# Kernel tuning notes

Measured on AMD Instinct MI355X. Metric: run time of the kernel, lower is better.

The kernel has to match this reference:

```python
import jax, jax.numpy as jnp
import numpy as np

SC = 19          # window stride/size (non-kitti)
K = 3 * SC       # 57, unfold kernel size
CH = 128         # chnn

def conv2d(x, w, b=None, pad=(0, 0)):
    y = jax.lax.conv_general_dilated(
        x, w, (1, 1), [(pad[0], pad[0]), (pad[1], pad[1])],
        dimension_numbers=('NCHW', 'OIHW', 'NCHW'))
    return y if b is None else y + b[None, :, None, None]

def unfold(x):
    # nn.Unfold(kernel_size=3*SC, padding=SC, stride=SC) -> [b, c, K*K, h_sc*w_sc]
    b, c, h, w = x.shape
    h_sc, w_sc = h // SC, w // SC
    xp = jnp.pad(x, ((0, 0), (0, 0), (SC, SC), (SC, SC)))
    ii = np.arange(h_sc)[:, None] * SC + np.arange(K)[None, :]
    jj = np.arange(w_sc)[:, None] * SC + np.arange(K)[None, :]
    p = xp[:, :, ii, :][:, :, :, :, jj]              # [b,c,h_sc,K,w_sc,K]
    return p.transpose(0, 1, 3, 5, 2, 4).reshape(b, c, K * K, h_sc * w_sc)

def to_windows(x):
    # [b,c,h,w] -> [b,c,h_sc*w_sc, SC*SC] (non-overlapping SCxSC windows)
    b, c, h, w = x.shape
    h_sc, w_sc = h // SC, w // SC
    return x.reshape(b, c, h_sc, SC, w_sc, SC).transpose(0, 1, 2, 4, 3, 5).reshape(b, c, h_sc * w_sc, SC * SC)

def fs_kernel(w_prelu, b, h, w):
    # geometric falloff kernel, separable in x/y: [b, K*K, L, SC*SC]
    a = w_prelu[0] * 0.02      # scp = 0.02
    half = 2.0 * SC            # half_ker
    crd = jnp.arange(K, dtype=jnp.float32)
    idx_x = SC + jnp.arange(w, dtype=jnp.float32) % SC
    idx_y = SC + jnp.arange(h, dtype=jnp.float32) % SC
    def falloff(d):
        v = d - half
        pre = jnp.where(v > 0, v, a * v)   # PReLU
        return jnp.maximum(1.0 - pre, 0.0) # -prelu + b(=1), clamped at 0
    ox = falloff(jnp.abs(crd[:, None] - idx_x[None, :]))  # [K, w]
    oy = falloff(jnp.abs(crd[:, None] - idx_y[None, :]))  # [K, h]
    ker = oy[:, None, :, None] * ox[None, :, None, :]      # [Ky, Kx, h, w]
    ker = jnp.broadcast_to(ker[None], (b, K, K, h, w)).reshape(b, K * K, h, w)
    return to_windows(ker)

def kpa(feat_ci, feat_mi, w_qk, w_v, gamma, w_prelu):
    b, c, h_in, w_in = feat_mi.shape
    x_pad = SC - w_in % SC
    y_pad = SC - h_in % SC
    pad4 = ((0, 0), (0, 0), (0, y_pad), (0, x_pad))
    feat_c = jnp.pad(feat_ci, pad4)
    feat_m = jnp.pad(feat_mi, pad4)
    h, w = h_in + y_pad, w_in + x_pad
    h_sc, w_sc = h // SC, w // SC
    # validity mask -> additive -99 bias for padded keys/queries
    fm = jnp.pad(jnp.ones((1, 1, h_in, w_in), feat_mi.dtype), pad4)
    fm_k = unfold(fm)                                  # [1,1,K^2,L]
    fm_q = to_windows(fm)                              # [1,1,L,SC^2]
    am = (fm_k[:, 0, :, :, None] * fm_q[:, 0, None, :, :] - 1.0) * 99.0
    # itr == 0 path: compute attention
    qk = conv2d(feat_c, w_qk)
    feat_q, feat_k = qk[:, :c], qk[:, c:]
    feat_k = unfold(feat_k) * (c ** -0.5)              # [b,c,K^2,L]
    feat_q = to_windows(feat_q)                        # [b,c,L,SC^2]
    attn = jnp.einsum('bckn,bcns->bkns', feat_k, feat_q) + am
    attn = jax.nn.softmax(fs_kernel(w_prelu, b, h, w) * attn, axis=1)
    feat_v = unfold(conv2d(feat_m, w_v))               # [b,c,K^2,L]
    feat_r = jnp.einsum('bkns,bckn->bcns', attn, feat_v)  # [b,c,L,SC^2]
    feat_r = feat_r.reshape(b, c, h_sc, w_sc, SC, SC).transpose(0, 1, 2, 4, 3, 5).reshape(b, c, h, w)
    return feat_mi + feat_r[:, :, :h_in, :w_in] * gamma[0]

def sep_conv_gru(h, x, wz1, bz1, wr1, br1, wq1, bq1, wz2, bz2, wr2, br2, wq2, bq2):
    hx = jnp.concatenate([h, x], 1)
    z = jax.nn.sigmoid(conv2d(hx, wz1, bz1, (0, 2)))
    r = jax.nn.sigmoid(conv2d(hx, wr1, br1, (0, 2)))
    q = jnp.tanh(conv2d(jnp.concatenate([r * h, x], 1), wq1, bq1, (0, 2)))
    h = (1 - z) * h + z * q
    hx = jnp.concatenate([h, x], 1)
    z = jax.nn.sigmoid(conv2d(hx, wz2, bz2, (2, 0)))
    r = jax.nn.sigmoid(conv2d(hx, wr2, br2, (2, 0)))
    q = jnp.tanh(conv2d(jnp.concatenate([r * h, x], 1), wq2, bq2, (2, 0)))
    return (1 - z) * h + z * q

PARAM_SHAPES = [
    ('w_cor1', (256, 324, 1, 1)), ('b_cor1', (256,)), ('w_cor2', (192, 256, 3, 3)), ('b_cor2', (192,)),
    ('w_flo1', (128, 2, 7, 7)), ('b_flo1', (128,)), ('w_flo2', (64, 128, 3, 3)), ('b_flo2', (64,)),
    ('w_mo', (126, 256, 3, 3)), ('b_mo', (126,)),
    ('w_qk', (256, 128, 1, 1)), ('w_v', (128, 128, 1, 1)),
    ('wz1', (128, 512, 1, 5)), ('bz1', (128,)), ('wr1', (128, 512, 1, 5)), ('br1', (128,)),
    ('wq1', (128, 512, 1, 5)), ('bq1', (128,)),
    ('wz2', (128, 512, 5, 1)), ('bz2', (128,)), ('wr2', (128, 512, 5, 1)), ('br2', (128,)),
    ('wq2', (128, 512, 5, 1)), ('bq2', (128,)),
    ('w_f1', (256, 128, 3, 3)), ('b_f1', (256,)), ('w_f2', (2, 256, 3, 3)), ('b_f2', (2,)),
    ('w_m1', (256, 128, 3, 3)), ('b_m1', (256,)), ('w_m2', (576, 256, 1, 1)), ('b_m2', (576,)),
]

def setup_inputs() -> dict:
    key = jax.random.key(0)
    B, H, W = 2, 55, 128
    ks = jax.random.split(key, len(PARAM_SHAPES) + 4)
    inp = {
        'net': jax.random.normal(ks[0], (B, CH, H, W), jnp.float32),
        'inp': jax.random.normal(ks[1], (B, CH, H, W), jnp.float32),
        'corr': jax.random.normal(ks[2], (B, 324, H, W), jnp.float32),
        'flow': jax.random.normal(ks[3], (B, 2, H, W), jnp.float32),
    }
    for i, (name, shp) in enumerate(PARAM_SHAPES):
        fan_in = int(np.prod(shp[1:])) if len(shp) > 1 else shp[0]
        scale = 1.0 / np.sqrt(fan_in) if len(shp) > 1 else 0.01
        inp[name] = scale * jax.random.normal(ks[4 + i], shp, jnp.float32)
    inp['gamma'] = jnp.array([0.5], jnp.float32)            # nonzero so KPA contributes
    inp['w_prelu'] = jnp.array([1.0 / 28.0], jnp.float32)    # 1 / h_k, h_k = (3*SC-1)/2
    inp['itr'] = 0
    return inp

def reference(net, inp, corr, flow, w_cor1, b_cor1, w_cor2, b_cor2, w_flo1, b_flo1, w_flo2, b_flo2, w_mo, b_mo, w_qk, w_v, wz1, bz1, wr1, br1, wq1, bq1, wz2, bz2, wr2, br2, wq2, bq2, w_f1, b_f1, w_f2, b_f2, w_m1, b_m1, w_m2, b_m2, gamma, w_prelu, itr):
    # _mo_enc
    fc = jax.nn.relu(conv2d(corr, w_cor1, b_cor1))
    fc = jax.nn.relu(conv2d(fc, w_cor2, b_cor2, (1, 1)))
    ff = jax.nn.relu(conv2d(flow, w_flo1, b_flo1, (3, 3)))
    ff = jax.nn.relu(conv2d(ff, w_flo2, b_flo2, (1, 1)))
    fm = jax.nn.relu(conv2d(jnp.concatenate([fc, ff], 1), w_mo, b_mo, (1, 1)))
    feat_mo = jnp.concatenate([fm, flow], 1)           # [b,128,h,w]
    # KPA attention (itr == 0)
    feat_moa = kpa(inp, feat_mo, w_qk, w_v, gamma, w_prelu)
    x = jnp.concatenate([inp, feat_mo, feat_moa], 1)   # [b,384,h,w]
    net = sep_conv_gru(net, x, wz1, bz1, wr1, br1, wq1, bq1, wz2, bz2, wr2, br2, wq2, bq2)
    d = jax.nn.relu(conv2d(net, w_f1, b_f1, (1, 1)))
    delta_flow = conv2d(d, w_f2, b_f2, (1, 1))
    m = jax.nn.relu(conv2d(net, w_m1, b_m1, (1, 1)))
    mask = 0.25 * conv2d(m, w_m2, b_m2)
    return net, mask, delta_flow
```

## Files before the change

kernel.cpp:

```cpp
#include <hip/hip_runtime.h>
#include <hip/hip_bf16.h>

typedef __bf16 bf16;
typedef __attribute__((ext_vector_type(8))) __bf16 v8bf;
typedef __attribute__((ext_vector_type(4))) float f32x4;
typedef __attribute__((ext_vector_type(16))) float f32x16;

#define HH 55
#define WW 128
#define HWP 7040
#define BHW 14080
#define QS 0.08838834764831845f
#define LOG2E 1.4426950408889634f

__device__ __forceinline__ void g2l16(const bf16* g, bf16* l){
  __builtin_amdgcn_global_load_lds(
      (const __attribute__((address_space(1))) void*)g,
      (__attribute__((address_space(3))) void*)l, 16, 0, 0);
}

#define NCV 17
__device__ const int PK_CinSrc[NCV] = {324,256,128,256,128,128,512,512,512,512,512,512,128,128,256,256,98};
__device__ const int PK_Kc[NCV]     = {384,256,128,256,128,128,512,512,512,512,512,512,128,128,256,256,128};
__device__ const int PK_ntap[NCV]   = {1,9,9,9,1,1,5,5,5,5,5,5,9,9,9,1,1};
__device__ const int PK_Ctot[NCV]   = {256,256,128,128,256,128,256,256,128,256,256,128,512,512,128,640,128};
__device__ const int PK_coB[NCV]    = {0,0,0,0,0,0,0,128,0,0,128,0,0,256,0,0,0};
__device__ const int PK_dst[NCV]    = {0,98304,688128,835584,1130496,1163264,1179648,1179648,
  1835008,2162688,2162688,2818048,3145728,3145728,3735552,4030464,4194304};
__device__ const int PKD_cum[NCV+1] = {0,98304,540672,614400,904704,937472,953856,
  1281536,1609216,1936896,2264576,2592256,2919936,3214848,3509760,3514368,3661824,3678208};
__device__ const int PKD_Co[NCV]    = {256,192,64,126,256,128,128,128,128,128,128,128,256,256,2,576,128};

__device__ const int PB_off[15]={0,256,512,640,1152,1280,1408,1536,1664,1792,1920,2176,2432,2560,3200};
__device__ const int PB_cnt[15]={256,192,64,126,128,128,128,128,128,128,256,256,2,576,128};

struct W17 { const float* w[17]; };
struct B15 { const float* b[15]; };

struct XP {
  W17 wp; B15 bp;
  const float *net, *inp, *corr, *flow;
  bf16 *Bp; float *bias;
  bf16 *hx; float *hcur; bf16 *corr_cl; bf16 *im2c;
};

__global__ __launch_bounds__(256) void init_k(XP X){
  __shared__ float T[64][65];
  int bid = blockIdx.x;
  const int t = threadIdx.x;
  if (bid < 14368){
    int idx = bid*256 + t;
    int c = 0;
    while (idx >= PKD_cum[c+1]) ++c;
    int local = idx - PKD_cum[c];
    if (c == 16){
      int co = local >> 7, k = local & 127;
      if (k < 98)
        X.Bp[PK_dst[16] + co*128 + k] = (bf16)X.wp.w[16][co*98 + (k&1)*49 + (k>>1)];
      return;
    }
    int Kc = PK_Kc[c];
    int CKc = PKD_Co[c]*Kc;
    int tap = local / CKc;
    int rem = local - tap*CKc;
    int co = rem / Kc;
    int ci = rem - co*Kc;
    int cs = PK_CinSrc[c];
    if (ci < cs){
      float v = X.wp.w[c][(co*cs + ci)*PK_ntap[c] + tap];
      if (c == 4 && co < 128) v *= QS;
      X.Bp[PK_dst[c] + (tap*PK_Ctot[c] + PK_coB[c] + co)*Kc + ci] = (bf16)v;
    }
    return;
  }
  bid -= 14368;
  if (bid < 880){
    int pt = bid%110, ct = (bid/110)&3, b = bid/440;
    const float* src = (ct < 2) ? X.net : X.inp;
    int c0s = (ct & 1)*64;
    int cbase = (ct < 2) ? 0 : 128;
    int p0 = pt*64;
    int pj = t & 63, cr4 = t >> 6;
#pragma unroll
    for (int i=0;i<16;++i)
      T[cr4 + i*4][pj] = src[((size_t)b*128 + c0s + cr4 + i*4)*HWP + p0 + pj];
    __syncthreads();
    int cj = t & 63, pr4 = t >> 6;
#pragma unroll
    for (int i=0;i<16;++i){
      int pp = p0 + pr4 + i*4;
      float v = T[cj][pr4 + i*4];
      X.hx[((size_t)(b*HWP+pp))*512 + cbase + c0s + cj] = (bf16)v;
      if (ct < 2) X.hcur[((size_t)(b*HWP+pp))*128 + c0s + cj] = v;
    }
    return;
  }
  bid -= 880;
  if (bid < 1320){
    int pt = bid%110, ct = (bid/110)%6, b = bid/660;
    int p0 = pt*64, c0s = ct*64;
    int pj = t & 63, cr4 = t >> 6;
#pragma unroll
    for (int i=0;i<16;++i){
      int c = c0s + cr4 + i*4;
      float v = 0.f;
      if (c < 324) v = X.corr[((size_t)b*324 + c)*HWP + p0 + pj];
      T[cr4 + i*4][pj] = v;
    }
    __syncthreads();
    int cj = t & 63, pr4 = t >> 6;
#pragma unroll
    for (int i=0;i<16;++i){
      int pp = p0 + pr4 + i*4;
      int cc = c0s + cj;
      X.corr_cl[((size_t)(b*HWP+pp))*384 + cc] = (bf16)T[cj][pr4 + i*4];
    }
    return;
  }
  bid -= 1320;
  if (bid < 110){
    int i = bid*256 + t;
    int c = i & 1, p = i >> 1;
    int b = p / HWP, pix = p - b*HWP;
    X.hx[(size_t)p*512 + 382 + c] = (bf16)X.flow[(b*2+c)*HWP + pix];
    return;
  }
  bid -= 110;
  if (bid < 7040){
    int i = bid*256 + t;
    int k = i & 127, p = i >> 7;
    int b = p / HWP, pix = p - b*HWP, y = pix >> 7, x = pix & 127;
    float v = 0.f;
    if (k < 98){
      int tap = k >> 1, c2 = k & 1, kh = tap/7, kw = tap - 7*(tap/7);
      int yy = y + kh - 3, xx = x + kw - 3;
      if ((unsigned)yy < 55u && (unsigned)xx < 128u) v = X.flow[(b*2+c2)*HWP + yy*128 + xx];
    }
    X.im2c[i] = (bf16)v;
    return;
  }
  for (int e=0;e<15;++e)
    for (int o=t; o<PB_cnt[e]; o+=256)
      X.bias[PB_off[e]+o] = X.bp.b[e][o];
}

__global__ __launch_bounds__(256) void transp_v(
    const bf16* __restrict__ src, bf16* __restrict__ dst)
{
  int pt = blockIdx.x, ct = blockIdx.y, b = blockIdx.z;
  __shared__ unsigned short T[64][66];
  int t = threadIdx.x;
  int p0 = pt*64, c0s = ct*64;
  int cj = t & 63, pr4 = t >> 6;
#pragma unroll
  for (int i=0;i<16;++i){
    int pp = p0 + pr4 + i*4;
    T[cj][pr4 + i*4] = ((const unsigned short*)src)[((size_t)(b*HWP+pp))*128 + c0s + cj];
  }
  __syncthreads();
  int pj = t & 63, cr4 = t >> 6;
#pragma unroll
  for (int i=0;i<16;++i){
    int cc = c0s + cr4 + i*4;
    ((unsigned short*)dst)[((size_t)(b*128 + cc))*HWP + p0 + pj] = T[cr4 + i*4][pj];
  }
}

struct GP {
  const bf16* A; const bf16* A2;
  const bf16* Bp; const float* bias;
  void* outp; const float* auxZ; float* auxH; float* auxN;
  int Astride, A2stride, Asplit;
  int outCtot, outC0, Nvalid, Kc, CtotPad, tapcode, act, outmode, ntiles, ntOff;
  float scale;
};

__global__ __launch_bounds__(256) void gemm_conv(GP ga, GP gb, const bf16* __restrict__ zp)
{
  const int Mt = blockIdx.x;
  int nt = blockIdx.y;
  const bool useB = (nt >= ga.ntiles);
  if (useB) nt -= ga.ntiles;
  const bf16* A        = useB ? gb.A : ga.A;
  const bf16* A2       = useB ? gb.A2 : ga.A2;
  const bf16* Bp       = useB ? gb.Bp : ga.Bp;
  const float* bias    = useB ? gb.bias : ga.bias;
  void* outp           = useB ? gb.outp : ga.outp;
  const float* auxZ    = useB ? gb.auxZ : ga.auxZ;
  float* auxH          = useB ? gb.auxH : ga.auxH;
  float* auxN          = useB ? gb.auxN : ga.auxN;
  const int Astride    = useB ? gb.Astride : ga.Astride;
  const int A2stride   = useB ? gb.A2stride : ga.A2stride;
  const int Asplit     = useB ? gb.Asplit : ga.Asplit;
  const int outCtot    = useB ? gb.outCtot : ga.outCtot;
  const int outC0      = useB ? gb.outC0 : ga.outC0;
  const int Nvalid     = useB ? gb.Nvalid : ga.Nvalid;
  const int Kc         = useB ? gb.Kc : ga.Kc;
  const int CtotPad    = useB ? gb.CtotPad : ga.CtotPad;
  const int tapcode    = useB ? gb.tapcode : ga.tapcode;
  const int act        = useB ? gb.act : ga.act;
  const int outmode    = useB ? gb.outmode : ga.outmode;
  const int ntOff      = useB ? gb.ntOff : ga.ntOff;
  const float scale    = useB ? gb.scale : ga.scale;

  const int bimg = Mt/110;
  const int rem = Mt - bimg*110;
  const int yy0 = rem >> 1;
  const int xh  = (rem & 1) << 6;
  const int tid = threadIdx.x;
  const int lane = tid & 63, wave = tid >> 6;
  const int wm = wave >> 1, wn = wave & 1;
  const int lr = lane & 15, lq2 = lane >> 4;

  __shared__ __align__(16) bf16 Al[2][4096];
  __shared__ __align__(16) bf16 Bl[2][8192];

  f32x4 acc[2][4];
#pragma unroll
  for (int m=0;m<2;++m)
#pragma unroll
    for (int n=0;n<4;++n) acc[m][n] = (f32x4){0.f,0.f,0.f,0.f};

  const int ntap = (tapcode==0) ? 1 : (tapcode==1 ? 9 : 5);
  const int nsteps = ntap*(Kc>>6);

  const int srow = tid >> 3;
  const int sc   = tid & 7;

#define STAGE(BUF, T, KC) { \
    int ddy, ddx; \
    if (tapcode==0){ ddy=0; ddx=0; } \
    else if (tapcode==1){ ddy=(T)/3-1; ddx=(T)-3*((T)/3)-1; } \
    else if (tapcode==2){ ddy=0; ddx=(T)-2; } \
    else { ddy=(T)-2; ddx=0; } \
    int ysrc = yy0 + ddy; \
    bool yok = (unsigned)ysrc < 55u; \
    const bf16* Abase; int Astr; \
    if ((KC) < Asplit){ Astr = A2stride; \
      Abase = A2 + (size_t)((bimg*55+ysrc)*128)*Astr + (KC); } \
    else { Astr = Astride; \
      Abase = A + (size_t)((bimg*55+ysrc)*128)*Astr + (KC); } \
    _Pragma("unroll") \
    for (int is=0; is<2; ++is){ \
      int r = is*32 + srow; \
      int cc = sc ^ (r&7); \
      int gx = xh + r + ddx; \
      const bf16* srcp = (yok && (unsigned)gx < 128u) ? \
          (Abase + (size_t)gx*Astr + cc*8) : (zp + cc*8); \
      g2l16(srcp, &Al[BUF][is*2048 + wave*512]); \
    } \
    const bf16* Bt = Bp + (size_t)((T)*CtotPad + (nt+ntOff)*128)*Kc + (KC); \
    _Pragma("unroll") \
    for (int is=0; is<4; ++is){ \
      int r = is*32 + srow; \
      int cc = sc ^ (r&7); \
      g2l16(Bt + (size_t)r*Kc + cc*8, &Bl[BUF][is*2048 + wave*512]); \
    } }

  STAGE(0, 0, 0);
  __syncthreads();

  int tcur = 0, kcc = 0;
  for (int si=0; si<nsteps; ++si){
    int kn = kcc + 64, tn = tcur;
    if (kn == Kc){ kn = 0; tn = tcur + 1; }
    if (si + 1 < nsteps){ STAGE((si+1)&1, tn, kn); }
    __builtin_amdgcn_sched_barrier(0);
    kcc = kn; tcur = tn;
    const bf16* Ac = Al[si&1];
    const bf16* Bc = Bl[si&1];
#pragma unroll
    for (int kk=0; kk<2; ++kk){
      v8bf af[2], bfr[4];
#pragma unroll
      for (int m=0;m<2;++m){
        int row = wm*32 + m*16 + lr;
        af[m] = *(const v8bf*)(Ac + row*64 + (((kk*4+lq2) ^ (row&7))<<3));
      }
#pragma unroll
      for (int n=0;n<4;++n){
        int row = wn*64 + n*16 + lr;
        bfr[n] = *(const v8bf*)(Bc + row*64 + (((kk*4+lq2) ^ (row&7))<<3));
      }
#pragma unroll
      for (int m=0;m<2;++m)
#pragma unroll
        for (int n=0;n<4;++n)
          acc[m][n] = __builtin_amdgcn_mfma_f32_16x16x32_bf16(af[m], bfr[n], acc[m][n], 0,0,0);
    }
    __syncthreads();
  }
#undef STAGE

  const size_t pixbase = (size_t)(bimg*55 + yy0)*128 + xh;
  if (outmode == 0){
    bf16* Ost = (bf16*)Al;
#pragma unroll
    for (int nn=0; nn<4; ++nn){
      int colL = wn*64 + nn*16 + lr;
      float bvl = bias[(nt+ntOff)*128 + colL];
#pragma unroll
      for (int m=0;m<2;++m){
        int rowx = wm*32 + m*16 + lq2*4;
        f32x4 v = acc[m][nn];
#pragma unroll
        for (int r=0;r<4;++r){
          float vv = v[r] + bvl;
          if (act==1)      vv = fmaxf(vv, 0.f);
          else if (act==2) vv = 1.f/(1.f+__expf(-vv));
          else if (act==3) vv = tanhf(vv);
          vv *= scale;
          int row = rowx + r;
          int pch = (colL>>3) ^ (row & 7);
          Ost[row*128 + (pch<<3) + (colL&7)] = (bf16)vv;
        }
      }
    }
    __syncthreads();
    {
      int rowl = tid >> 2, seg = tid & 3;
      size_t p = pixbase + rowl;
      bf16* dstp = (bf16*)outp + p*outCtot + outC0 + (nt+ntOff)*128 + seg*32;
      const bf16* srcr = Ost + rowl*128;
      int cb = (nt+ntOff)*128 + seg*32;
#pragma unroll
      for (int k2=0;k2<4;++k2){
        int pch = (seg*4 + k2) ^ (rowl & 7);
        int cog = cb + k2*8;
        if (cog + 8 <= Nvalid)
          *(uint4*)(dstp + k2*8) = *(const uint4*)(srcr + (pch<<3));
        else if (cog < Nvalid){
          const bf16* s8 = srcr + (pch<<3);
          for (int e=0; e<Nvalid-cog; ++e) dstp[k2*8+e] = s8[e];
        }
      }
    }
  } else if (outmode == 2){
    float* Ost2 = (float*)Bl;
#pragma unroll
    for (int nn=0; nn<4; ++nn){
      int chL = wn*64 + nn*16 + lr;
      float bvl = bias[(nt+ntOff)*128 + chL];
#pragma unroll
      for (int m=0;m<2;++m){
        int rowx = wm*32 + m*16 + lq2*4;
        f32x4 v = acc[m][nn];
#pragma unroll
        for (int r=0;r<4;++r){
          float vv = v[r] + bvl;
          if (act==1)      vv = fmaxf(vv, 0.f);
          else if (act==2) vv = 1.f/(1.f+__expf(-vv));
          else if (act==3) vv = tanhf(vv);
          Ost2[chL*64 + rowx + r] = vv*scale;
        }
      }
    }
    __syncthreads();
    {
      int ch = tid >> 1, half = tid & 1;
      int cog = (nt+ntOff)*128 + ch;
      if (cog < Nvalid){
        float* dstp = (float*)outp + ((size_t)bimg*outCtot + outC0 + cog)*HWP
                    + yy0*128 + xh + half*32;
        const float* srcr = Ost2 + ch*64 + half*32;
#pragma unroll
        for (int k2=0;k2<8;++k2)
          *(uint4*)(dstp + k2*4) = *(const uint4*)(srcr + k2*4);
      }
    }
  } else {
#pragma unroll
    for (int nn=0; nn<4; ++nn){
      int cog = (nt+ntOff)*128 + wn*64 + nn*16 + lr;
      float bvl = bias[cog];
      bool cok = cog < Nvalid;
#pragma unroll
      for (int m=0;m<2;++m){
        int rowx = wm*32 + m*16 + lq2*4;
        f32x4 v = acc[m][nn];
#pragma unroll
        for (int r=0;r<4;++r){
          float vv = v[r] + bvl;
          if (act==1)      vv = fmaxf(vv, 0.f);
          else if (act==2) vv = 1.f/(1.f+__expf(-vv));
          else if (act==3) vv = tanhf(vv);
          vv *= scale;
          if (cok){
            int prow = rowx + r;
            size_t p = pixbase + prow;
            if (outmode==1) ((float*)outp)[p*outCtot + outC0 + cog] = vv;
            else if (outmode==3){
              int c = cog & 127;
              ((bf16*)outp)[p*128 + c] = (bf16)(vv * auxH[p*128 + c]);
            } else {
              int c = cog;
              float z  = auxZ[p*128 + c];
              float h0 = auxH[p*128 + c];
              float hn = (1.f - z)*h0 + z*vv;
              auxH[p*128 + c] = hn;
              ((bf16*)outp)[p*512 + c] = (bf16)hn;
              if (auxN){
                int pixloc = (int)(p - (size_t)bimg*HWP);
                auxN[((size_t)bimg*128 + c)*HWP + pixloc] = hn;
              }
            }
          }
        }
      }
    }
  }
}

__global__ __launch_bounds__(256) void gemm_n16(
    const bf16* __restrict__ A, int Astride,
    const bf16* __restrict__ Bp, const float* __restrict__ bias,
    float* __restrict__ outp, int outCtot, int Kc, int CtotPad)
{
  const int Mt = blockIdx.x;
  const int bimg = Mt/110;
  const int rem = Mt - bimg*110;
  const int yy0 = rem >> 1;
  const int xh  = (rem & 1) << 6;
  const int tid = threadIdx.x;
  const int wave = tid >> 6, lane = tid & 63;
  const int lr = lane & 15, lq2 = lane >> 4;

  __shared__ __align__(16) bf16 Al[4][2560];
  __shared__ __align__(16) bf16 Bl[4][640];
  __shared__ float Rd[4][1024];

  bf16* Alw = Al[wave];
  bf16* Blw = Bl[wave];

  f32x4 acc[4];
#pragma unroll
  for (int m=0;m<4;++m) acc[m] = (f32x4){0.f,0.f,0.f,0.f};

  const int brw = lane >> 2, bc = lane & 3;
  uint4 av[4]; uint4 bv;

#define PFN(SI) { \
    int T_ = (SI) >> 3, KC = ((SI)&7)*32; \
    int ddy = T_/3 - 1, ddx = T_ - 3*(T_/3) - 1; \
    int ysrc = yy0 + ddy; int gx = xh + lane + ddx; \
    bool ok = (unsigned)ysrc < 55u && (unsigned)gx < 128u; \
    const bf16* Ap = A + (size_t)((bimg*55+ysrc)*128 + gx)*Astride + KC; \
    av[0] = ok ? *(const uint4*)(Ap)      : make_uint4(0,0,0,0); \
    av[1] = ok ? *(const uint4*)(Ap + 8)  : make_uint4(0,0,0,0); \
    av[2] = ok ? *(const uint4*)(Ap + 16) : make_uint4(0,0,0,0); \
    av[3] = ok ? *(const uint4*)(Ap + 24) : make_uint4(0,0,0,0); \
    bv = *(const uint4*)(Bp + (size_t)(T_*CtotPad + brw)*Kc + KC + bc*8); }

  const int s0 = wave*18;
  PFN(s0);
  for (int si=s0; si<s0+18; ++si){
    *(uint4*)(Alw + lane*40 + 0)  = av[0];
    *(uint4*)(Alw + lane*40 + 8)  = av[1];
    *(uint4*)(Alw + lane*40 + 16) = av[2];
    *(uint4*)(Alw + lane*40 + 24) = av[3];
    *(uint4*)(Blw + brw*40 + bc*8) = bv;
    if (si + 1 < s0+18) PFN(si+1);
    v8bf bq = *(const v8bf*)(Blw + lr*40 + lq2*8);
#pragma unroll
    for (int m=0;m<4;++m){
      v8bf af = *(const v8bf*)(Alw + (m*16 + lr)*40 + lq2*8);
      acc[m] = __builtin_amdgcn_mfma_f32_16x16x32_bf16(af, bq, acc[m], 0,0,0);
    }
  }
#undef PFN

#pragma unroll
  for (int m=0;m<4;++m)
    *(f32x4*)&Rd[wave][lane*16 + m*4] = acc[m];
  __syncthreads();
  if (wave == 0 && lr < 2){
    float bvl = bias[lr];
#pragma unroll
    for (int m=0;m<4;++m)
#pragma unroll
      for (int r=0;r<4;++r){
        int ix = lane*16 + m*4 + r;
        float s = Rd[0][ix] + Rd[1][ix] + Rd[2][ix] + Rd[3][ix];
        int row = m*16 + lq2*4 + r;
        outp[((size_t)bimg*outCtot + lr)*HWP + yy0*128 + xh + row] = s + bvl;
      }
  }
}

__global__ __launch_bounds__(256,1) void attn_k(
    const bf16* __restrict__ QK, const bf16* __restrict__ Vt,
    bf16* __restrict__ hx,
    const float* __restrict__ gammap, const float* __restrict__ wprelup)
{
  __shared__ __align__(16) float SM[16640];
  const int tid = threadIdx.x;
  const int wv = tid >> 6, lane = tid & 63;
  const int lq = lane & 31, hi = lane >> 5;
  const int blk0 = blockIdx.x;
  const int blk = (blk0 & 7)*63 + (blk0 >> 3);
  const int qt = blk % 12;
  const int n  = (blk/12) % 21;
  const int b  = blk / 252;
  const int hs = n/7, wd = n - 7*hs;
  const int y0 = (hs-1)*19, x0 = (wd-1)*19;
  const int rylo = max(0, y0), ryhi = min(54, y0+56);
  const int rxlo = max(0, x0), rxhi = min(127, x0+56);
  const int rxA  = rxlo & ~7;
  const int s = qt*32 + lq;
  const int sy = s/19, sx = s - sy*19;
  const int qy = y0 + 19 + sy, qx = x0 + 19 + sx;
  const int qpix = (b*55 + min(qy,54))*128 + min(qx,127);
  const float a = wprelup[0]*0.02f;
  const float qyf = (float)qy;

  bf16* Kl = (bf16*)SM + wv*8192;
  bf16* Vl = Kl + 4096;

  v8bf qf[8];
#pragma unroll
  for (int ks=0; ks<8; ++ks)
    qf[ks] = *(const v8bf*)(QK + (size_t)qpix*256 + ks*16 + hi*8);

  float fx0[16], fx1[16];
  unsigned msk0 = 0, msk1 = 0;
  {
    float dxq0 = (float)(rxA - qx);
    int xl0 = rxlo - rxA, xm0 = rxhi - rxA;
#pragma unroll
    for (int r=0;r<16;++r){
      int Ri = (r&3) + 8*(r>>2) + 4*hi;
      float dxv = fabsf(dxq0 + (float)Ri) - 38.f;
      fx0[r] = fmaxf(1.f - fmaxf(dxv, a*dxv), 0.f);
      if (Ri >= xl0 && Ri <= xm0) msk0 |= 1u<<r;
      float dxv1 = fabsf(dxq0 + 32.f + (float)Ri) - 38.f;
      fx1[r] = fmaxf(1.f - fmaxf(dxv1, a*dxv1), 0.f);
      int Ri1 = Ri + 32;
      if (Ri1 >= xl0 && Ri1 <= xm0) msk1 |= 1u<<r;
    }
  }

  f32x16 acc[4];
#pragma unroll
  for (int nf=0; nf<4; ++nf)
#pragma unroll
    for (int r=0;r<16;++r) acc[nf][r] = 0.f;
  float m2 = -40.f, den = 0.f;

  const int nry = (ryhi - rylo - wv)/4 + 1;
  const int nit = nry*2;

#define ISSUE_K(RY, RX) { int pixK = (b*55+(RY))*128 + (RX); \
  _Pragma("unroll") \
  for (int i=0;i<8;++i){ \
    int key = i*4 + (lane>>4); int cs = (lane&15) ^ (key&7); \
    g2l16(QK + (size_t)(pixK+key)*256 + 128 + cs*8, Kl + i*512); } }
#define ISSUE_V(RY, RX) { \
  _Pragma("unroll") \
  for (int i=0;i<8;++i){ \
    int ch = i*16 + (lane>>2); int cs = (lane&3) ^ ((ch>>1)&3); \
    g2l16(Vt + (size_t)(b*128+ch)*HWP + (RY)*128 + (RX) + cs*8, Vl + i*512); } }

  ISSUE_K(rylo + wv, rxA);

  for (int it=0; it<nit; ++it){
    const int ry  = rylo + wv + (it>>1)*4;
    const int tpar = it & 1;
    asm volatile("s_waitcnt lgkmcnt(0)" ::: "memory");
    __builtin_amdgcn_sched_barrier(0);
    asm volatile("s_waitcnt vmcnt(0)" ::: "memory");
    __builtin_amdgcn_sched_barrier(0);
    ISSUE_V(ry, rxA + tpar*32);
    __builtin_amdgcn_sched_barrier(0);

    f32x16 Cs;
#pragma unroll
    for (int r=0;r<16;++r) Cs[r] = 0.f;
#pragma unroll
    for (int ks=0; ks<8; ++ks){
      v8bf kf = *(const v8bf*)(Kl + lq*128 + (((ks*2+hi) ^ (lq&7))<<3));
      Cs = __builtin_amdgcn_mfma_f32_32x32x16_bf16(kf, qf[ks], Cs, 0,0,0);
    }
    float pr[16];
    {
      float dyv = fabsf((float)ry - qyf) - 38.f;
      float fy = fmaxf(1.f - fmaxf(dyv, a*dyv), 0.f);
      float fyk = fy * LOG2E;
      unsigned mk = tpar ? msk1 : msk0;
      float l2v[16]; float tmax = -1e30f;
#pragma unroll
      for (int r=0;r<16;++r){
        float fx = tpar ? fx1[r] : fx0[r];
        float lv = fyk * fx * Cs[r];
        lv = ((mk>>r)&1u) ? lv : -1e30f;
        l2v[r] = lv;
        tmax = fmaxf(tmax, lv);
      }
      tmax = fmaxf(tmax, __shfl_xor(tmax, 32));
      if (__any(tmax > m2 + 11.f)){
        float m2n = fmaxf(m2, tmax);
        float sc = exp2f(m2 - m2n);
        den *= sc;
#pragma unroll
        for (int r=0;r<16;++r){
          float scr = __shfl(sc, (r&3) + 8*(r>>2) + 4*hi);
          acc[0][r]*=scr; acc[1][r]*=scr; acc[2][r]*=scr; acc[3][r]*=scr;
        }
        m2 = m2n;
      }
#pragma unroll
      for (int r=0;r<16;++r){
        pr[r] = exp2f(l2v[r] - m2);
        den += pr[r];
      }
    }
    asm volatile("s_waitcnt lgkmcnt(0)" ::: "memory");
    __builtin_amdgcn_sched_barrier(0);
    asm volatile("s_waitcnt vmcnt(0)" ::: "memory");
    __builtin_amdgcn_sched_barrier(0);
    if (it + 1 < nit){
      int ryn = rylo + wv + ((it+1)>>1)*4;
      ISSUE_K(ryn, rxA + ((it+1)&1)*32);
      __builtin_amdgcn_sched_barrier(0);
    }
    float po[8], po2[8];
#pragma unroll
    for (int r=0;r<8;++r) po[r]  = __shfl_xor(pr[r],   32);
#pragma unroll
    for (int r=0;r<8;++r) po2[r] = __shfl_xor(pr[r+8], 32);
    v8bf pa0, pa1;
#pragma unroll
    for (int j=0;j<4;++j){
      pa0[j]   = (bf16)(hi ? po[j+4]  : pr[j]);
      pa0[j+4] = (bf16)(hi ? pr[j+4]  : po[j]);
      pa1[j]   = (bf16)(hi ? po2[j+4] : pr[j+8]);
      pa1[j+4] = (bf16)(hi ? pr[j+12] : po2[j]);
    }
#pragma unroll
    for (int nf=0; nf<4; ++nf){
      int ch = nf*32 + lq;
      int sw = (lq>>1)&3;
      v8bf v0 = *(const v8bf*)(Vl + ch*32 + ((hi     ^ sw)<<3));
      v8bf v1 = *(const v8bf*)(Vl + ch*32 + (((2+hi) ^ sw)<<3));
      acc[nf] = __builtin_amdgcn_mfma_f32_32x32x16_bf16(pa0, v0, acc[nf], 0,0,0);
      acc[nf] = __builtin_amdgcn_mfma_f32_32x32x16_bf16(pa1, v1, acc[nf], 0,0,0);
    }
  }
#undef ISSUE_K
#undef ISSUE_V
  den += __shfl_xor(den, 32);

  float* Osh = SM;
  float* Msh = SM + 16384;
  float* Dsh = SM + 16512;
  __syncthreads();
#pragma unroll
  for (int nf=0; nf<4; ++nf)
#pragma unroll
    for (int r=0;r<16;++r)
      Osh[(wv*32 + (r&3) + 8*(r>>2) + 4*hi)*128 + nf*32 + lq] = acc[nf][r];
  if (hi == 0){ Msh[wv*32 + lq] = m2; Dsh[wv*32 + lq] = den; }
  __syncthreads();

  int q = tid >> 3, co = (tid & 7)*16;
  float m0 = Msh[q], m1 = Msh[32+q], mm2 = Msh[64+q], m3 = Msh[96+q];
  float M = fmaxf(fmaxf(m0,m1), fmaxf(mm2,m3));
  float s0 = exp2f(m0-M), s1 = exp2f(m1-M), s2 = exp2f(mm2-M), s3 = exp2f(m3-M);
  int ss = qt*32 + q;
  float dent = s0*Dsh[q] + s1*Dsh[32+q] + s2*Dsh[64+q] + s3*Dsh[96+q];
  int sy2 = ss/19, sx2 = ss - sy2*19;
  int qy2 = y0 + 19 + sy2, qx2 = x0 + 19 + sx2;
  if (ss < 361 && qy2 < 55 && qx2 < 128){
    size_t pix = (size_t)(b*55+qy2)*128 + qx2;
    float g = gammap[0] / dent;
#pragma unroll
    for (int c=0;c<16;++c){
      float o = s0*Osh[q*128+co+c] + s1*Osh[(32+q)*128+co+c]
              + s2*Osh[(64+q)*128+co+c] + s3*Osh[(96+q)*128+co+c];
      float fm = (float)hx[pix*512 + 256 + co + c];
      hx[pix*512 + 384 + co + c] = (bf16)(fm + o*g);
    }
  }
}

static inline GP mkgp(const bf16* A, int Astride, const bf16* Bp, const float* bias,
                      void* outp, int outCtot, int outC0, int Nvalid, int Kc, int CtotPad,
                      int tapcode, int act, int outmode, float scale, int ntiles){
  GP g{};
  g.A=A; g.A2=A; g.Astride=Astride; g.A2stride=Astride; g.Asplit=0;
  g.Bp=Bp; g.bias=bias; g.outp=outp; g.auxZ=nullptr; g.auxH=nullptr; g.auxN=nullptr;
  g.outCtot=outCtot; g.outC0=outC0; g.Nvalid=Nvalid; g.Kc=Kc; g.CtotPad=CtotPad;
  g.tapcode=tapcode; g.act=act; g.outmode=outmode; g.ntiles=ntiles; g.ntOff=0;
  g.scale=scale;
  return g;
}

extern "C" void kernel_launch(void* const* d_in, const int* in_sizes, int n_in,
                              void* d_out, int out_size, void* d_ws, size_t ws_size,
                              hipStream_t stream) {
  const float* net   = (const float*)d_in[0];
  const float* inp   = (const float*)d_in[1];
  const float* corr  = (const float*)d_in[2];
  const float* flow  = (const float*)d_in[3];
  const float* w_cor1=(const float*)d_in[4];  const float* b_cor1=(const float*)d_in[5];
  const float* w_cor2=(const float*)d_in[6];  const float* b_cor2=(const float*)d_in[7];
  const float* w_flo1=(const float*)d_in[8];  const float* b_flo1=(const float*)d_in[9];
  const float* w_flo2=(const float*)d_in[10]; const float* b_flo2=(const float*)d_in[11];
  const float* w_mo  =(const float*)d_in[12]; const float* b_mo  =(const float*)d_in[13];
  const float* w_qk  =(const float*)d_in[14];
  const float* w_v   =(const float*)d_in[15];
  const float* wz1=(const float*)d_in[16]; const float* bz1=(const float*)d_in[17];
  const float* wr1=(const float*)d_in[18]; const float* br1=(const float*)d_in[19];
  const float* wq1=(const float*)d_in[20]; const float* bq1=(const float*)d_in[21];
  const float* wz2=(const float*)d_in[22]; const float* bz2=(const float*)d_in[23];
  const float* wr2=(const float*)d_in[24]; const float* br2=(const float*)d_in[25];
  const float* wq2=(const float*)d_in[26]; const float* bq2=(const float*)d_in[27];
  const float* w_f1=(const float*)d_in[28]; const float* b_f1=(const float*)d_in[29];
  const float* w_f2=(const float*)d_in[30]; const float* b_f2=(const float*)d_in[31];
  const float* w_m1=(const float*)d_in[32]; const float* b_m1=(const float*)d_in[33];
  const float* w_m2=(const float*)d_in[34]; const float* b_m2=(const float*)d_in[35];
  const float* gamma  =(const float*)d_in[36];
  const float* w_prelu=(const float*)d_in[37];

  float* ws = (float*)d_ws;
  bf16* hx     = (bf16*)ws;
  bf16* BPp    = (bf16*)(ws + 3604480);
  float* BIASp = ws + 5709824;
  const bf16* zp = (const bf16*)(ws + 5713152);
  const size_t S0 = 5713216;
  bf16* corr_cl = (bf16*)(ws + S0);
  bf16* fc1o    = (bf16*)(ws + S0 + 2703360);
  bf16* catB    = (bf16*)(ws + S0 + 4505600);
  bf16* ff1o    = (bf16*)(ws + S0 + 6307840);
  bf16* im2c    = (bf16*)(ws + S0 + 7208960);
  float* hcur   = ws + S0 + 8110080;
  bf16* QKb    = (bf16*)(ws + S0);
  bf16* Vb     = (bf16*)(ws + S0 + 1810432);
  bf16* Vt     = (bf16*)(ws + S0 + 2711552);
  float* zb    = ws + S0;
  bf16* rhb    = (bf16*)(ws + S0 + 3604480);
  bf16* dm     = (bf16*)(ws + S0);

  float* out_net  = (float*)d_out;
  float* out_mask = out_net + 1802240;
  float* out_df   = out_net + 9912320;

  dim3 blk(256);

  hipMemsetAsync(ws + 3604480, 0, (size_t)8434944, stream);
  XP X{};
  const float* wl[17] = {w_cor1,w_cor2,w_flo2,w_mo,w_qk,w_v,wz1,wr1,wq1,wz2,wr2,wq2,w_f1,w_m1,w_f2,w_m2,w_flo1};
  const float* bl[15] = {b_cor1,b_cor2,b_flo2,b_mo,bz1,br1,bq1,bz2,br2,bq2,b_f1,b_m1,b_f2,b_m2,b_flo1};
  for (int i=0;i<17;++i) X.wp.w[i]=wl[i];
  for (int i=0;i<15;++i) X.bp.b[i]=bl[i];
  X.net=net; X.inp=inp; X.corr=corr; X.flow=flow;
  X.Bp=BPp; X.bias=BIASp; X.hx=hx; X.hcur=hcur; X.corr_cl=corr_cl; X.im2c=im2c;
  init_k<<<dim3(14368+880+1320+110+7040+1),blk,0,stream>>>(X);

  GP g0{};

  {
    GP a = mkgp(corr_cl,384, BPp+0,       BIASp+0,    fc1o,256,0,256, 384,256, 0,1,0,1.f, 2);
    GP b = mkgp(im2c,128,    BPp+4194304, BIASp+3200, ff1o,128,0,128, 128,128, 0,1,0,1.f, 1);
    gemm_conv<<<dim3(220,3),blk,0,stream>>>(a, b, zp);
  }
  {
    GP a = mkgp(fc1o,256,    BPp+98304,   BIASp+256,  catB,256,0,192, 256,256, 1,1,0,1.f, 2);
    GP b = mkgp(ff1o,128,    BPp+688128,  BIASp+512,  catB,256,192,64,128,128, 1,1,0,1.f, 1);
    gemm_conv<<<dim3(220,3),blk,0,stream>>>(a, b, zp);
  }
  {
    GP a = mkgp(catB,256,    BPp+835584,  BIASp+640,  hx,  512,256,126,256,128, 1,1,0,1.f, 1);
    gemm_conv<<<dim3(220,1),blk,0,stream>>>(a, g0, zp);
  }

  {
    GP a = mkgp(hx+128,512,  BPp+1130496, BIASp+768,  QKb, 256,0,256, 128,256, 0,0,0,1.f, 2);
    GP b = mkgp(hx+256,512,  BPp+1163264, BIASp+1024, Vb,  128,0,128, 128,128, 0,0,0,1.f, 1);
    gemm_conv<<<dim3(220,3),blk,0,stream>>>(a, b, zp);
  }
  transp_v<<<dim3(110,2,2),blk,0,stream>>>(Vb, Vt);
  attn_k<<<dim3(504),blk,0,stream>>>(QKb, Vt, hx, gamma, w_prelu);

  {
    GP a = mkgp(hx,512,      BPp+1179648, BIASp+1152, zb,  128,0,128, 512,256, 2,2,1,1.f, 1);
    GP b = mkgp(hx,512,      BPp+1179648, BIASp+1152, rhb, 0,0,256,   512,256, 2,2,3,1.f, 1);
    b.ntOff = 1; b.auxH = hcur;
    gemm_conv<<<dim3(220,2),blk,0,stream>>>(a, b, zp);
  }
  {
    GP a = mkgp(hx,512,      BPp+1835008, BIASp+1408, hx,  0,0,128,   512,128, 2,3,4,1.f, 1);
    a.A2 = rhb; a.A2stride = 128; a.Asplit = 128;
    a.auxZ = zb; a.auxH = hcur; a.auxN = nullptr;
    gemm_conv<<<dim3(220,1),blk,0,stream>>>(a, g0, zp);
  }

  {
    GP a = mkgp(hx,512,      BPp+2162688, BIASp+1536, zb,  128,0,128, 512,256, 3,2,1,1.f, 1);
    GP b = mkgp(hx,512,      BPp+2162688, BIASp+1536, rhb, 0,0,256,   512,256, 3,2,3,1.f, 1);
    b.ntOff = 1; b.auxH = hcur;
    gemm_conv<<<dim3(220,2),blk,0,stream>>>(a, b, zp);
  }
  {
    GP a = mkgp(hx,512,      BPp+2818048, BIASp+1792, hx,  0,0,128,   512,128, 3,3,4,1.f, 1);
    a.A2 = rhb; a.A2stride = 128; a.Asplit = 128;
    a.auxZ = zb; a.auxH = hcur; a.auxN = out_net;
    gemm_conv<<<dim3(220,1),blk,0,stream>>>(a, g0, zp);
  }

  {
    GP a = mkgp(hx,512,      BPp+3145728, BIASp+1920, dm,  512,0,512, 128,512, 1,1,0,1.f, 4);
    gemm_conv<<<dim3(220,4),blk,0,stream>>>(a, g0, zp);
  }
  gemm_n16 <<<dim3(220),blk,0,stream>>>(dm,512,   BPp+3735552, BIASp+2432, out_df, 2, 256,128);
  {
    GP a = mkgp(dm+256,512,  BPp+4030464, BIASp+2560, out_mask,576,0,576,256,640, 0,0,2,0.25f, 5);
    gemm_conv<<<dim3(220,5),blk,0,stream>>>(a, g0, zp);
  }
}
```

Baseline: 544.9 us.

## Split GRU q-conv to overlap x-part with z/r gates and fold flow head

```diff
diff --git a/kernel.cpp b/kernel.cpp
--- a/kernel.cpp
+++ b/kernel.cpp
@@ -19,17 +19,21 @@
       (__attribute__((address_space(3))) void*)l, 16, 0, 0);
 }
 
-#define NCV 17
-__device__ const int PK_CinSrc[NCV] = {324,256,128,256,128,128,512,512,512,512,512,512,128,128,256,256,98};
-__device__ const int PK_Kc[NCV]     = {384,256,128,256,128,128,512,512,512,512,512,512,128,128,256,256,128};
-__device__ const int PK_ntap[NCV]   = {1,9,9,9,1,1,5,5,5,5,5,5,9,9,9,1,1};
-__device__ const int PK_Ctot[NCV]   = {256,256,128,128,256,128,256,256,128,256,256,128,512,512,128,640,128};
-__device__ const int PK_coB[NCV]    = {0,0,0,0,0,0,0,128,0,0,128,0,0,256,0,0,0};
+#define NCV 19
+__device__ const int PK_srcCS[NCV]  = {324,256,128,256,128,128,512,512,512,512,512,512,128,128,256,256,98,512,512};
+__device__ const int PK_csv[NCV]    = {324,256,128,256,128,128,512,512,128,512,512,128,128,128,256,256,98,384,384};
+__device__ const int PK_srcOff[NCV] = {0,0,0,0,0,0,0,0,0,0,0,0,0,0,0,0,0,128,128};
+__device__ const int PK_wsrc[NCV]   = {0,1,2,3,4,5,6,7,8,9,10,11,12,13,14,15,16,8,11};
+__device__ const int PK_Kc[NCV]     = {384,256,128,256,128,128,512,512,128,512,512,128,128,128,256,256,128,384,384};
+__device__ const int PK_ntap[NCV]   = {1,9,9,9,1,1,5,5,5,5,5,5,9,9,9,1,1,5,5};
+__device__ const int PK_Ctot[NCV]   = {256,256,128,128,256,128,256,256,128,256,256,128,512,512,128,640,128,128,128};
+__device__ const int PK_coB[NCV]    = {0,0,0,0,0,0,0,128,0,0,128,0,0,256,0,0,0,0,0};
 __device__ const int PK_dst[NCV]    = {0,98304,688128,835584,1130496,1163264,1179648,1179648,
-  1835008,2162688,2162688,2818048,3145728,3145728,3735552,4030464,4194304};
+  1835008,2162688,2162688,2818048,3145728,3145728,3735552,4030464,4194304,1916928,2899968};
 __device__ const int PKD_cum[NCV+1] = {0,98304,540672,614400,904704,937472,953856,
-  1281536,1609216,1936896,2264576,2592256,2919936,3214848,3509760,3514368,3661824,3678208};
-__device__ const int PKD_Co[NCV]    = {256,192,64,126,256,128,128,128,128,128,128,128,256,256,2,576,128};
+  1281536,1609216,1691136,2018816,2346496,2428416,2723328,3018240,3022848,3170304,
+  3186688,3432448,3678208};
+__device__ const int PKD_Co[NCV]    = {256,192,64,126,256,128,128,128,128,128,128,128,256,256,2,576,128,128,128};
 
 __device__ const int PB_off[15]={0,256,512,640,1152,1280,1408,1536,1664,1792,1920,2176,2432,2560,3200};
 __device__ const int PB_cnt[15]={256,192,64,126,128,128,128,128,128,128,256,256,2,576,128};
@@ -65,9 +69,8 @@
     int rem = local - tap*CKc;
     int co = rem / Kc;
     int ci = rem - co*Kc;
-    int cs = PK_CinSrc[c];
-    if (ci < cs){
-      float v = X.wp.w[c][(co*cs + ci)*PK_ntap[c] + tap];
+    if (ci < PK_csv[c]){
+      float v = X.wp.w[PK_wsrc[c]][(co*PK_srcCS[c] + PK_srcOff[c] + ci)*PK_ntap[c] + tap];
       if (c == 4 && co < 128) v *= QS;
       X.Bp[PK_dst[c] + (tap*PK_Ctot[c] + PK_coB[c] + co)*Kc + ci] = (bf16)v;
     }
@@ -169,39 +172,42 @@
 struct GP {
   const bf16* A; const bf16* A2;
   const bf16* Bp; const float* bias;
-  void* outp; const float* auxZ; float* auxH; float* auxN;
+  void* outp; const float* auxZ; float* auxH; float* auxN; const float* auxQ;
   int Astride, A2stride, Asplit;
   int outCtot, outC0, Nvalid, Kc, CtotPad, tapcode, act, outmode, ntiles, ntOff;
   float scale;
 };
 
-__global__ __launch_bounds__(256) void gemm_conv(GP ga, GP gb, const bf16* __restrict__ zp)
+__global__ __launch_bounds__(256) void gemm_conv(GP ga, GP gb, GP gc, const bf16* __restrict__ zp)
 {
   const int Mt = blockIdx.x;
   int nt = blockIdx.y;
-  const bool useB = (nt >= ga.ntiles);
-  if (useB) nt -= ga.ntiles;
-  const bf16* A        = useB ? gb.A : ga.A;
-  const bf16* A2       = useB ? gb.A2 : ga.A2;
-  const bf16* Bp       = useB ? gb.Bp : ga.Bp;
-  const float* bias    = useB ? gb.bias : ga.bias;
-  void* outp           = useB ? gb.outp : ga.outp;
-  const float* auxZ    = useB ? gb.auxZ : ga.auxZ;
-  float* auxH          = useB ? gb.auxH : ga.auxH;
-  float* auxN          = useB ? gb.auxN : ga.auxN;
-  const int Astride    = useB ? gb.Astride : ga.Astride;
-  const int A2stride   = useB ? gb.A2stride : ga.A2stride;
-  const int Asplit     = useB ? gb.Asplit : ga.Asplit;
-  const int outCtot    = useB ? gb.outCtot : ga.outCtot;
-  const int outC0      = useB ? gb.outC0 : ga.outC0;
-  const int Nvalid     = useB ? gb.Nvalid : ga.Nvalid;
-  const int Kc         = useB ? gb.Kc : ga.Kc;
-  const int CtotPad    = useB ? gb.CtotPad : ga.CtotPad;
-  const int tapcode    = useB ? gb.tapcode : ga.tapcode;
-  const int act        = useB ? gb.act : ga.act;
-  const int outmode    = useB ? gb.outmode : ga.outmode;
-  const int ntOff      = useB ? gb.ntOff : ga.ntOff;
-  const float scale    = useB ? gb.scale : ga.scale;
+  GP g;
+  if (nt < ga.ntiles){ g = ga; }
+  else if (nt < ga.ntiles + gb.ntiles){ g = gb; nt -= ga.ntiles; }
+  else { g = gc; nt -= ga.ntiles + gb.ntiles; }
+  const bf16* A        = g.A;
+  const bf16* A2       = g.A2;
+  const bf16* Bp       = g.Bp;
+  const float* bias    = g.bias;
+  void* outp           = g.outp;
+  const float* auxZ    = g.auxZ;
+  float* auxH          = g.auxH;
+  float* auxN          = g.auxN;
+  const float* auxQ    = g.auxQ;
+  const int Astride    = g.Astride;
+  const int A2stride   = g.A2stride;
+  const int Asplit     = g.Asplit;
+  const int outCtot    = g.outCtot;
+  const int outC0      = g.outC0;
+  const int Nvalid     = g.Nvalid;
+  const int Kc         = g.Kc;
+  const int CtotPad    = g.CtotPad;
+  const int tapcode    = g.tapcode;
+  const int act        = g.act;
+  const int outmode    = g.outmode;
+  const int ntOff      = g.ntOff;
+  const float scale    = g.scale;
 
   const int bimg = Mt/110;
   const int rem = Mt - bimg*110;
@@ -380,14 +386,15 @@
         f32x4 v = acc[m][nn];
 #pragma unroll
         for (int r=0;r<4;++r){
+          int prow = rowx + r;
+          size_t p = pixbase + prow;
           float vv = v[r] + bvl;
+          if (outmode==4 && auxQ) vv += auxQ[p*128 + cog];
           if (act==1)      vv = fmaxf(vv, 0.f);
           else if (act==2) vv = 1.f/(1.f+__expf(-vv));
           else if (act==3) vv = tanhf(vv);
           vv *= scale;
           if (cok){
-            int prow = rowx + r;
-            size_t p = pixbase + prow;
             if (outmode==1) ((float*)outp)[p*outCtot + outC0 + cog] = vv;
             else if (outmode==3){
               int c = cog & 127;
@@ -411,82 +418,6 @@
   }
 }
 
-__global__ __launch_bounds__(256) void gemm_n16(
-    const bf16* __restrict__ A, int Astride,
-    const bf16* __restrict__ Bp, const float* __restrict__ bias,
-    float* __restrict__ outp, int outCtot, int Kc, int CtotPad)
-{
-  const int Mt = blockIdx.x;
-  const int bimg = Mt/110;
-  const int rem = Mt - bimg*110;
-  const int yy0 = rem >> 1;
-  const int xh  = (rem & 1) << 6;
-  const int tid = threadIdx.x;
-  const int wave = tid >> 6, lane = tid & 63;
-  const int lr = lane & 15, lq2 = lane >> 4;
-
-  __shared__ __align__(16) bf16 Al[4][2560];
-  __shared__ __align__(16) bf16 Bl[4][640];
-  __shared__ float Rd[4][1024];
-
-  bf16* Alw = Al[wave];
-  bf16* Blw = Bl[wave];
-
-  f32x4 acc[4];
-#pragma unroll
-  for (int m=0;m<4;++m) acc[m] = (f32x4){0.f,0.f,0.f,0.f};
-
-  const int brw = lane >> 2, bc = lane & 3;
-  uint4 av[4]; uint4 bv;
-
-#define PFN(SI) { \
-    int T_ = (SI) >> 3, KC = ((SI)&7)*32; \
-    int ddy = T_/3 - 1, ddx = T_ - 3*(T_/3) - 1; \
-    int ysrc = yy0 + ddy; int gx = xh + lane + ddx; \
-    bool ok = (unsigned)ysrc < 55u && (unsigned)gx < 128u; \
-    const bf16* Ap = A + (size_t)((bimg*55+ysrc)*128 + gx)*Astride + KC; \
-    av[0] = ok ? *(const uint4*)(Ap)      : make_uint4(0,0,0,0); \
-    av[1] = ok ? *(const uint4*)(Ap + 8)  : make_uint4(0,0,0,0); \
-    av[2] = ok ? *(const uint4*)(Ap + 16) : make_uint4(0,0,0,0); \
-    av[3] = ok ? *(const uint4*)(Ap + 24) : make_uint4(0,0,0,0); \
-    bv = *(const uint4*)(Bp + (size_t)(T_*CtotPad + brw)*Kc + KC + bc*8); }
-
-  const int s0 = wave*18;
-  PFN(s0);
-  for (int si=s0; si<s0+18; ++si){
-    *(uint4*)(Alw + lane*40 + 0)  = av[0];
-    *(uint4*)(Alw + lane*40 + 8)  = av[1];
-    *(uint4*)(Alw + lane*40 + 16) = av[2];
-    *(uint4*)(Alw + lane*40 + 24) = av[3];
-    *(uint4*)(Blw + brw*40 + bc*8) = bv;
-    if (si + 1 < s0+18) PFN(si+1);
-    v8bf bq = *(const v8bf*)(Blw + lr*40 + lq2*8);
-#pragma unroll
-    for (int m=0;m<4;++m){
-      v8bf af = *(const v8bf*)(Alw + (m*16 + lr)*40 + lq2*8);
-      acc[m] = __builtin_amdgcn_mfma_f32_16x16x32_bf16(af, bq, acc[m], 0,0,0);
-    }
-  }
-#undef PFN
-
-#pragma unroll
-  for (int m=0;m<4;++m)
-    *(f32x4*)&Rd[wave][lane*16 + m*4] = acc[m];
-  __syncthreads();
-  if (wave == 0 && lr < 2){
-    float bvl = bias[lr];
-#pragma unroll
-    for (int m=0;m<4;++m)
-#pragma unroll
-      for (int r=0;r<4;++r){
-        int ix = lane*16 + m*4 + r;
-        float s = Rd[0][ix] + Rd[1][ix] + Rd[2][ix] + Rd[3][ix];
-        int row = m*16 + lq2*4 + r;
-        outp[((size_t)bimg*outCtot + lr)*HWP + yy0*128 + xh + row] = s + bvl;
-      }
-  }
-}
-
 __global__ __launch_bounds__(256,1) void attn_k(
     const bf16* __restrict__ QK, const bf16* __restrict__ Vt,
     bf16* __restrict__ hx,
@@ -496,8 +427,7 @@
   const int tid = threadIdx.x;
   const int wv = tid >> 6, lane = tid & 63;
   const int lq = lane & 31, hi = lane >> 5;
-  const int blk0 = blockIdx.x;
-  const int blk = (blk0 & 7)*63 + (blk0 >> 3);
+  const int blk = blockIdx.x;
   const int qt = blk % 12;
   const int n  = (blk/12) % 21;
   const int b  = blk / 252;
@@ -687,7 +617,8 @@
                       int tapcode, int act, int outmode, float scale, int ntiles){
   GP g{};
   g.A=A; g.A2=A; g.Astride=Astride; g.A2stride=Astride; g.Asplit=0;
-  g.Bp=Bp; g.bias=bias; g.outp=outp; g.auxZ=nullptr; g.auxH=nullptr; g.auxN=nullptr;
+  g.Bp=Bp; g.bias=bias; g.outp=outp;
+  g.auxZ=nullptr; g.auxH=nullptr; g.auxN=nullptr; g.auxQ=nullptr;
   g.outCtot=outCtot; g.outC0=outC0; g.Nvalid=Nvalid; g.Kc=Kc; g.CtotPad=CtotPad;
   g.tapcode=tapcode; g.act=act; g.outmode=outmode; g.ntiles=ntiles; g.ntOff=0;
   g.scale=scale;
@@ -726,7 +657,8 @@
   bf16* BPp    = (bf16*)(ws + 3604480);
   float* BIASp = ws + 5709824;
   const bf16* zp = (const bf16*)(ws + 5713152);
-  const size_t S0 = 5713216;
+  float* ZB0   = ws + 5713216;
+  const size_t S0 = 5713344;
   bf16* corr_cl = (bf16*)(ws + S0);
   bf16* fc1o    = (bf16*)(ws + S0 + 2703360);
   bf16* catB    = (bf16*)(ws + S0 + 4505600);
@@ -737,6 +669,7 @@
   bf16* Vb     = (bf16*)(ws + S0 + 1810432);
   bf16* Vt     = (bf16*)(ws + S0 + 2711552);
   float* zb    = ws + S0;
+  float* qpart = ws + S0 + 1802240;
   bf16* rhb    = (bf16*)(ws + S0 + 3604480);
   bf16* dm     = (bf16*)(ws + S0);
 
@@ -746,7 +679,7 @@
 
   dim3 blk(256);
 
-  hipMemsetAsync(ws + 3604480, 0, (size_t)8434944, stream);
+  hipMemsetAsync(ws + 3604480, 0, (size_t)8435456, stream);
   XP X{};
   const float* wl[17] = {w_cor1,w_cor2,w_flo2,w_mo,w_qk,w_v,wz1,wr1,wq1,wz2,wr2,wq2,w_f1,w_m1,w_f2,w_m2,w_flo1};
   const float* bl[15] = {b_cor1,b_cor2,b_flo2,b_mo,bz1,br1,bq1,bz2,br2,bq2,b_f1,b_m1,b_f2,b_m2,b_flo1};
@@ -761,22 +694,22 @@
   {
     GP a = mkgp(corr_cl,384, BPp+0,       BIASp+0,    fc1o,256,0,256, 384,256, 0,1,0,1.f, 2);
     GP b = mkgp(im2c,128,    BPp+4194304, BIASp+3200, ff1o,128,0,128, 128,128, 0,1,0,1.f, 1);
-    gemm_conv<<<dim3(220,3),blk,0,stream>>>(a, b, zp);
+    gemm_conv<<<dim3(220,3),blk,0,stream>>>(a, b, g0, zp);
   }
   {
     GP a = mkgp(fc1o,256,    BPp+98304,   BIASp+256,  catB,256,0,192, 256,256, 1,1,0,1.f, 2);
     GP b = mkgp(ff1o,128,    BPp+688128,  BIASp+512,  catB,256,192,64,128,128, 1,1,0,1.f, 1);
-    gemm_conv<<<dim3(220,3),blk,0,stream>>>(a, b, zp);
+    gemm_conv<<<dim3(220,3),blk,0,stream>>>(a, b, g0, zp);
   }
   {
     GP a = mkgp(catB,256,    BPp+835584,  BIASp+640,  hx,  512,256,126,256,128, 1,1,0,1.f, 1);
-    gemm_conv<<<dim3(220,1),blk,0,stream>>>(a, g0, zp);
+    gemm_conv<<<dim3(220,1),blk,0,stream>>>(a, g0, g0, zp);
   }
 
   {
     GP a = mkgp(hx+128,512,  BPp+1130496, BIASp+768,  QKb, 256,0,256, 128,256, 0,0,0,1.f, 2);
     GP b = mkgp(hx+256,512,  BPp+1163264, BIASp+1024, Vb,  128,0,128, 128,128, 0,0,0,1.f, 1);
-    gemm_conv<<<dim3(220,3),blk,0,stream>>>(a, b, zp);
+    gemm_conv<<<dim3(220,3),blk,0,stream>>>(a, b, g0, zp);
   }
   transp_v<<<dim3(110,2,2),blk,0,stream>>>(Vb, Vt);
   attn_k<<<dim3(504),blk,0,stream>>>(QKb, Vt, hx, gamma, w_prelu);
@@ -785,35 +718,35 @@
     GP a = mkgp(hx,512,      BPp+1179648, BIASp+1152, zb,  128,0,128, 512,256, 2,2,1,1.f, 1);
     GP b = mkgp(hx,512,      BPp+1179648, BIASp+1152, rhb, 0,0,256,   512,256, 2,2,3,1.f, 1);
     b.ntOff = 1; b.auxH = hcur;
-    gemm_conv<<<dim3(220,2),blk,0,stream>>>(a, b, zp);
-  }
-  {
-    GP a = mkgp(hx,512,      BPp+1835008, BIASp+1408, hx,  0,0,128,   512,128, 2,3,4,1.f, 1);
-    a.A2 = rhb; a.A2stride = 128; a.Asplit = 128;
-    a.auxZ = zb; a.auxH = hcur; a.auxN = nullptr;
-    gemm_conv<<<dim3(220,1),blk,0,stream>>>(a, g0, zp);
+    GP c = mkgp(hx+128,512,  BPp+1916928, ZB0,        qpart,128,0,128,384,128, 2,0,1,1.f, 1);
+    gemm_conv<<<dim3(220,3),blk,0,stream>>>(a, b, c, zp);
+  }
+  {
+    GP a = mkgp(rhb,128,     BPp+1835008, BIASp+1408, hx,  0,0,128,   128,128, 2,3,4,1.f, 1);
+    a.auxZ = zb; a.auxH = hcur; a.auxN = nullptr; a.auxQ = qpart;
+    gemm_conv<<<dim3(220,1),blk,0,stream>>>(a, g0, g0, zp);
   }
 
   {
     GP a = mkgp(hx,512,      BPp+2162688, BIASp+1536, zb,  128,0,128, 512,256, 3,2,1,1.f, 1);
     GP b = mkgp(hx,512,      BPp+2162688, BIASp+1536, rhb, 0,0,256,   512,256, 3,2,3,1.f, 1);
     b.ntOff = 1; b.auxH = hcur;
-    gemm_conv<<<dim3(220,2),blk,0,stream>>>(a, b, zp);
-  }
-  {
-    GP a = mkgp(hx,512,      BPp+2818048, BIASp+1792, hx,  0,0,128,   512,128, 3,3,4,1.f, 1);
-    a.A2 = rhb; a.A2stride = 128; a.Asplit = 128;
-    a.auxZ = zb; a.auxH = hcur; a.auxN = out_net;
-    gemm_conv<<<dim3(220,1),blk,0,stream>>>(a, g0, zp);
+    GP c = mkgp(hx+128,512,  BPp+2899968, ZB0,        qpart,128,0,128,384,128, 3,0,1,1.f, 1);
+    gemm_conv<<<dim3(220,3),blk,0,stream>>>(a, b, c, zp);
+  }
+  {
+    GP a = mkgp(rhb,128,     BPp+2818048, BIASp+1792, hx,  0,0,128,   128,128, 3,3,4,1.f, 1);
+    a.auxZ = zb; a.auxH = hcur; a.auxN = out_net; a.auxQ = qpart;
+    gemm_conv<<<dim3(220,1),blk,0,stream>>>(a, g0, g0, zp);
   }
 
   {
     GP a = mkgp(hx,512,      BPp+3145728, BIASp+1920, dm,  512,0,512, 128,512, 1,1,0,1.f, 4);
-    gemm_conv<<<dim3(220,4),blk,0,stream>>>(a, g0, zp);
-  }
-  gemm_n16 <<<dim3(220),blk,0,stream>>>(dm,512,   BPp+3735552, BIASp+2432, out_df, 2, 256,128);
+    gemm_conv<<<dim3(220,4),blk,0,stream>>>(a, g0, g0, zp);
+  }
   {
     GP a = mkgp(dm+256,512,  BPp+4030464, BIASp+2560, out_mask,576,0,576,256,640, 0,0,2,0.25f, 5);
-    gemm_conv<<<dim3(220,5),blk,0,stream>>>(a, g0, zp);
+    GP b = mkgp(dm,512,      BPp+3735552, BIASp+2432, out_df,  2,  0,2,  256,128, 1,0,2,1.f,   1);
+    gemm_conv<<<dim3(220,6),blk,0,stream>>>(a, b, g0, zp);
   }
 }
```

New measurement: 521.7 us. 4.3% less time.
